# Optimization experiments

Hardware: AMD Instinct MI355X
Metric: run time of the kernel (lower is better)

## Reference

```python
import jax, jax.numpy as jnp
import numpy as np

# CODABlocks (codomain attention) with per_channel_attention=True:
# token_codimension = head_codimension = 1, scale = 2, n_modes = [32, 32],
# mixer_modes = [16, 16], temperature = 1.0, instance_norm (affine) everywhere.
N_HEADS = 16
TEMPERATURE = 1.0
EPS = 1e-5

def _gelu(z):
    return jax.nn.gelu(z, approximate=False)  # matches torch F.gelu default (erf)

def instance_norm(x, g, b):
    # x: (B, C, H, W); normalize over spatial dims per (sample, channel), affine.
    mu = jnp.mean(x, axis=(-2, -1), keepdims=True)
    var = jnp.var(x, axis=(-2, -1), keepdims=True)
    return (x - mu) * jax.lax.rsqrt(var + EPS) * g[:, None, None] + b[:, None, None]

def conv1x1(x, w, b):
    return jnp.einsum('bihw,io->bohw', x, w) + b[None, :, None, None]

def fourier_resample(x, out_shape):
    # FFT-based spatial resampling (mode truncation / zero-pad), norm='forward'.
    if tuple(x.shape[-2:]) == tuple(out_shape):
        return x
    Ho, Wo = out_shape
    xft = jnp.fft.rfftn(x, axes=(-2, -1), norm='forward')
    out = jnp.zeros(x.shape[:-2] + (Ho, Wo // 2 + 1), dtype=xft.dtype)
    hk = min(x.shape[-2], Ho) // 2
    wk = min(xft.shape[-1], Wo // 2 + 1)
    out = out.at[..., :hk, :wk].set(xft[..., :hk, :wk])
    out = out.at[..., -hk:, :wk].set(xft[..., -hk:, :wk])
    return jnp.fft.irfftn(out, s=out_shape, axes=(-2, -1), norm='forward')

def spectral_conv(x, w, out_shape):
    # Truncated-mode spectral convolution (dense weights, equiv. to tucker rank=1.0).
    # w: (Cin, Cout, 2*mh, mw, 2) -> complex weight on kept Fourier modes.
    wc = w[..., 0] + 1j * w[..., 1]
    mh = wc.shape[2] // 2
    mw = wc.shape[3]
    Ho, Wo = out_shape
    xft = jnp.fft.rfftn(x, axes=(-2, -1), norm='forward')   # (B, Cin, H, W//2+1)
    top = jnp.einsum('bihw,iohw->bohw', xft[:, :, :mh, :mw], wc[:, :, :mh])
    bot = jnp.einsum('bihw,iohw->bohw', xft[:, :, -mh:, :mw], wc[:, :, mh:])
    out_ft = jnp.zeros((x.shape[0], wc.shape[1], Ho, Wo // 2 + 1), dtype=xft.dtype)
    out_ft = out_ft.at[:, :, :mh, :mw].set(top)
    out_ft = out_ft.at[:, :, -mh:, :mw].set(bot)
    return jnp.fft.irfftn(out_ft, s=out_shape, axes=(-2, -1), norm='forward')

def fno_layer(x, spec_w, skip_w, skip_b, out_shape, norm=None, act=None):
    # One FNOBlocks layer: spectral conv + (resampled) linear skip, optional norm/act.
    xs = fourier_resample(conv1x1(x, skip_w, skip_b), out_shape)
    xf = spectral_conv(x, spec_w, out_shape)
    if norm is not None:
        xf = instance_norm(xf, *norm)
    y = xf + xs
    return act(y) if act is not None else y

def codano_forward(x, key_w, key_skip_w, key_skip_b, query_w, query_skip_w, query_skip_b, value_w, value_skip_w, value_skip_b, proj_w, proj_skip_w, proj_skip_b, norm1_g, norm1_b, attn_norm_g, attn_norm_b, norm2_g, norm2_b, mixer_w1, mixer_skip_w1, mixer_skip_b1, mixer_norm_g1, mixer_norm_b1, mixer_w2, mixer_skip_w2, mixer_skip_b2, mixer_norm_g2, mixer_norm_b2, mixer_out_g, mixer_out_b):
    b, t, H, W = x.shape   # token codim d = 1 -> channel dim == number of tokens
    tokens = x.reshape(b * t, 1, H, W)
    tokens_norm = instance_norm(tokens, norm1_g, norm1_b)
    Hs, Ws = H // 2, W // 2   # K, Q downsampled by scale = 2
    k = fno_layer(tokens_norm, key_w, key_skip_w, key_skip_b, (Hs, Ws))
    q = fno_layer(tokens_norm, query_w, query_skip_w, query_skip_b, (Hs, Ws))
    v = fno_layer(tokens_norm, value_w, value_skip_w, value_skip_b, (H, W))

    def heads_flat(z):
        hh, ww = z.shape[-2:]
        # (b*t, n_heads*d, h, w) -> (b, heads, t, d*h*w), d = 1
        return z.reshape(b, t, N_HEADS, hh * ww).transpose(0, 2, 1, 3)

    kf, qf, vf = heads_flat(k), heads_flat(q), heads_flat(v)
    scale = jnp.sqrt(jnp.asarray(kf.shape[-1], jnp.float32)) * TEMPERATURE
    dprod = jax.nn.softmax(jnp.einsum('bhtd,bhsd->bhts', qf, kf) / scale, axis=-1)
    attn = jnp.einsum('bhts,bhsd->bhtd', dprod, vf)      # (b, heads, t, H*W)
    attn = attn.transpose(0, 2, 1, 3).reshape(b * t, N_HEADS, H, W)
    # multi-head projection back to token codimension (n_heads -> 1)
    attn = fno_layer(attn, proj_w, proj_skip_w, proj_skip_b, (H, W))
    attn = instance_norm(attn + tokens, attn_norm_g, attn_norm_b)
    # permutation-equivariant mixer: 2 FNO layers shared across all tokens
    m = instance_norm(attn, norm2_g, norm2_b)
    m = fno_layer(m, mixer_w1, mixer_skip_w1, mixer_skip_b1, (H, W), norm=(mixer_norm_g1, mixer_norm_b1), act=_gelu)
    m = fno_layer(m, mixer_w2, mixer_skip_w2, mixer_skip_b2, (H, W), norm=(mixer_norm_g2, mixer_norm_b2))
    out = instance_norm(m, mixer_out_g, mixer_out_b) + attn
    return out.reshape(b, t, H, W)

def setup_inputs():
    key = jax.random.key(0)
    ks = list(jax.random.split(key, 32))
    f32 = jnp.float32
    def W_(k, shape, s=0.02):
        return (s * jax.random.normal(k, shape)).astype(f32)
    B, T, H, Wd = 4, 32, 128, 128
    mh_s, mw_s = 16, 9    # mixer_modes [16,16]: 2*(16//2) rows, 16//2+1 rfft cols
    mh_f, mw_f = 32, 17   # n_modes [32,32]
    return {
        'x': jax.random.normal(ks[0], (B, T, H, Wd), dtype=f32),
        'key_w': W_(ks[1], (1, N_HEADS, mh_s, mw_s, 2)),
        'key_skip_w': W_(ks[2], (1, N_HEADS), 0.5),
        'key_skip_b': W_(ks[3], (N_HEADS,)),
        'query_w': W_(ks[4], (1, N_HEADS, mh_s, mw_s, 2)),
        'query_skip_w': W_(ks[5], (1, N_HEADS), 0.5),
        'query_skip_b': W_(ks[6], (N_HEADS,)),
        'value_w': W_(ks[7], (1, N_HEADS, mh_s, mw_s, 2)),
        'value_skip_w': W_(ks[8], (1, N_HEADS), 0.5),
        'value_skip_b': W_(ks[9], (N_HEADS,)),
        'proj_w': W_(ks[10], (N_HEADS, 1, mh_f, mw_f, 2)),
        'proj_skip_w': W_(ks[11], (N_HEADS, 1), 0.25),
        'proj_skip_b': W_(ks[12], (1,)),
        'norm1_g': jnp.ones((1,), f32), 'norm1_b': jnp.zeros((1,), f32),
        'attn_norm_g': jnp.ones((1,), f32), 'attn_norm_b': jnp.zeros((1,), f32),
        'norm2_g': jnp.ones((1,), f32), 'norm2_b': jnp.zeros((1,), f32),
        'mixer_w1': W_(ks[13], (1, 1, mh_f, mw_f, 2)),
        'mixer_skip_w1': W_(ks[14], (1, 1), 0.5),
        'mixer_skip_b1': W_(ks[15], (1,)),
        'mixer_norm_g1': jnp.ones((1,), f32), 'mixer_norm_b1': jnp.zeros((1,), f32),
        'mixer_w2': W_(ks[16], (1, 1, mh_f, mw_f, 2)),
        'mixer_skip_w2': W_(ks[17], (1, 1), 0.5),
        'mixer_skip_b2': W_(ks[18], (1,)),
        'mixer_norm_g2': jnp.ones((1,), f32), 'mixer_norm_b2': jnp.zeros((1,), f32),
        'mixer_out_g': jnp.ones((1,), f32), 'mixer_out_b': jnp.zeros((1,), f32),
    }

def reference(x, key_w, key_skip_w, key_skip_b, query_w, query_skip_w, query_skip_b, value_w, value_skip_w, value_skip_b, proj_w, proj_skip_w, proj_skip_b, norm1_g, norm1_b, attn_norm_g, attn_norm_b, norm2_g, norm2_b, mixer_w1, mixer_skip_w1, mixer_skip_b1, mixer_norm_g1, mixer_norm_b1, mixer_w2, mixer_skip_w2, mixer_skip_b2, mixer_norm_g2, mixer_norm_b2, mixer_out_g, mixer_out_b):
    return codano_forward(x, key_w, key_skip_w, key_skip_b, query_w, query_skip_w, query_skip_b, value_w, value_skip_w, value_skip_b, proj_w, proj_skip_w, proj_skip_b, norm1_g, norm1_b, attn_norm_g, attn_norm_b, norm2_g, norm2_b, mixer_w1, mixer_skip_w1, mixer_skip_b1, mixer_norm_g1, mixer_norm_b1, mixer_w2, mixer_skip_w2, mixer_skip_b2, mixer_norm_g2, mixer_norm_b2, mixer_out_g, mixer_out_b)
```

## Files before the change

kernel.cpp:

```cpp
#include <hip/hip_runtime.h>
#include <cmath>

#define PI_F 3.14159265358979323846f
#define NTOK 128
#define NPIX 16384
#define NHEADS 16

__device__ __forceinline__ void block_reduce2(float& a, float& b){
  __shared__ float sa[4], sb[4];
  __syncthreads();
  for (int o=32;o>0;o>>=1){ a += __shfl_down(a,o); b += __shfl_down(b,o); }
  int w = threadIdx.x>>6, l = threadIdx.x&63;
  if (l==0){ sa[w]=a; sb[w]=b; }
  __syncthreads();
  a = sa[0]+sa[1]+sa[2]+sa[3];
  b = sb[0]+sb[1]+sb[2]+sb[3];
}

__device__ __forceinline__ float block_reduce1(float a){
  __shared__ float sa[4];
  __syncthreads();
  for (int o=32;o>0;o>>=1) a += __shfl_down(a,o);
  int w = threadIdx.x>>6, l = threadIdx.x&63;
  if (l==0) sa[w]=a;
  __syncthreads();
  return sa[0]+sa[1]+sa[2]+sa[3];
}

__device__ __forceinline__ float gelu_f(float y){
  return 0.5f*y*(1.f + erff(y*0.70710678118f));
}

__device__ __forceinline__ void affine_from(const float* __restrict__ ps, float g, float bb, int t,
                                            float& a, float& b0){
  float sum=0.f,sq=0.f;
  #pragma unroll
  for (int s=0;s<8;s++){ const float* p=ps+((size_t)t*8+s)*2; sum+=p[0]; sq+=p[1]; }
  const float iN=1.f/NPIX;
  float mu=sum*iN, var=sq*iN-mu*mu;
  a=rsqrtf(var+1e-5f)*g;
  b0=bb-mu*a;
}
__device__ __forceinline__ void scalA_from(const float* __restrict__ psA, float ag, float n2g, int t,
                                           float& muZ, float& aA, float& a0){
  float sum=0.f,sq=0.f;
  #pragma unroll
  for (int s=0;s<8;s++){ const float* p=psA+((size_t)t*8+s)*2; sum+=p[0]; sq+=p[1]; }
  const float iN=1.f/NPIX;
  muZ=sum*iN; float var=sq*iN-muZ*muZ;
  float inv=rsqrtf(var+1e-5f);
  aA=inv*ag;
  float var2=aA*aA*var;
  a0=aA*rsqrtf(var2+1e-5f)*n2g;
}
__device__ __forceinline__ void scalB_from(const float* __restrict__ psB, float mng1, int t,
                                           float& mu1, float& c1){
  float sum=0.f,sq=0.f;
  #pragma unroll
  for (int s=0;s<8;s++){ const float* p=psB+((size_t)t*8+s)*2; sum+=p[0]; sq+=p[1]; }
  const float iN=1.f/NPIX;
  mu1=sum*iN; float var=sq*iN-mu1*mu1;
  c1=rsqrtf(var+1e-5f)*mng1;
}
__device__ __forceinline__ void scalC_from(const float* __restrict__ psC, float mng2, float K, float sw,
                                           float outg, int t,
                                           float& mu2f, float& c2, float& mu3, float& c3){
  float sf=0.f,sfsq=0.f,sm=0.f,smsq=0.f,sx=0.f;
  #pragma unroll
  for (int s=0;s<8;s++){
    const float* p=psC+((size_t)t*8+s)*5;
    sf+=p[0]; sfsq+=p[1]; sm+=p[2]; smsq+=p[3]; sx+=p[4];
  }
  const float iN=1.f/NPIX;
  mu2f=sf*iN; float var2=sfsq*iN-mu2f*mu2f;
  c2=rsqrtf(var2+1e-5f)*mng2;
  float Em1=sm*iN, Em1sq=smsq*iN, Exm=sx*iN;
  float Em2=K+sw*Em1;
  float Em2sq = c2*c2*var2 + sw*sw*Em1sq + K*K
              + 2.f*c2*sw*(Exm - mu2f*Em1) + 2.f*K*sw*Em1;
  float var_m2=Em2sq-Em2*Em2;
  mu3=Em2;
  c3=rsqrtf(var_m2+1e-5f)*outg;
}

__global__ __launch_bounds__(256) void k_stats0(const float* __restrict__ x, float* __restrict__ pstat){
  int t=blockIdx.x, slab=blockIdx.y;
  const float* xs = x + (size_t)t*NPIX + slab*2048;
  float sum=0.f, sq=0.f;
  for (int i=threadIdx.x;i<2048;i+=256){ float v=xs[i]; sum+=v; sq+=v*v; }
  block_reduce2(sum,sq);
  if (threadIdx.x==0){ float* o=pstat+((size_t)t*8+slab)*2; o[0]=sum; o[1]=sq; }
}

__global__ __launch_bounds__(256) void k_colfft33(const float* __restrict__ x, const float* __restrict__ pstat0,
                          const float* __restrict__ n1g, const float* __restrict__ n1b,
                          float* __restrict__ A){
  __shared__ float rows[16*128];
  __shared__ float tw[128][2];
  int base = blockIdx.x*16;
  int t = base>>7;
  float a,b0; affine_from(pstat0, n1g[0], n1b[0], t, a, b0);
  for (int i=threadIdx.x;i<2048;i+=256) rows[i] = a*x[(size_t)base*128 + i] + b0;
  for (int p=threadIdx.x;p<128;p+=256){ float sn,cs; sincosf(-(2.f*PI_F/128.f)*(float)p,&sn,&cs); tw[p][0]=cs; tw[p][1]=sn; }
  __syncthreads();
  for (int e=threadIdx.x;e<16*33;e+=256){
    int r=e/33, c=e%33;
    const float* rp=rows+r*128;
    float re=0.f, im=0.f;
    for (int w=0;w<128;w++){
      int p=(c*w)&127;
      float v=rp[w];
      re+=v*tw[p][0]; im+=v*tw[p][1];
    }
    float* o=A+((size_t)(base+r)*33+c)*2; o[0]=re; o[1]=im;
  }
}

__global__ __launch_bounds__(256) void k_rowfft64(const float* __restrict__ A,
                          float* __restrict__ X64, float* __restrict__ X64h){
  int s=blockIdx.x, cg=blockIdx.y;
  int c0=cg*11;
  __shared__ float a[128][11][2];
  __shared__ float S[64][11][2];
  __shared__ float tw[128][2];
  for (int i=threadIdx.x;i<128*22;i+=256){
    int r=i/22, q=i%22;
    a[r][q>>1][q&1] = A[((size_t)(s*128+r)*33 + c0)*2 + q];
  }
  for (int p=threadIdx.x;p<128;p+=256){ float sn,cs; sincosf(-(2.f*PI_F/128.f)*(float)p,&sn,&cs); tw[p][0]=cs; tw[p][1]=sn; }
  __syncthreads();
  const float sc=1.f/16384.f;
  for (int e=threadIdx.x;e<64*11;e+=256){
    int i2=e/11, cl=e%11;
    int r=(i2<32)? i2 : i2+64;
    float re=0.f, im=0.f;
    for (int h=0;h<128;h++){
      int p=(r*h)&127;
      float cs=tw[p][0], sn=tw[p][1];
      float ar=a[h][cl][0], ai=a[h][cl][1];
      re+=ar*cs-ai*sn; im+=ar*sn+ai*cs;
    }
    S[i2][cl][0]=re*sc; S[i2][cl][1]=im*sc;
  }
  __syncthreads();
  for (int e=threadIdx.x;e<64*11;e+=256){
    int r=e/11, cl=e%11; int c=c0+cl;
    float vr=S[r][cl][0], vi=S[r][cl][1];
    float* o=X64+((size_t)s*(64*33)+r*33+c)*2; o[0]=vr; o[1]=vi;
    float hr=vr, hi=vi;
    if (c==0 || c==32){
      int pr=(64-r)&63;
      hr=0.5f*(vr+S[pr][cl][0]);
      hi=0.5f*(vi-S[pr][cl][1]);
    }
    float* oh=X64h+((size_t)s*(64*33)+r*33+c)*2; oh[0]=hr; oh[1]=hi;
  }
}

__global__ __launch_bounds__(256) void k_Ue(const float* __restrict__ X64h, float* __restrict__ Ue){
  int b=blockIdx.x, t=blockIdx.y, sg=blockIdx.z;
  __shared__ float2 xt[2112];
  const float2* src = (const float2*)(X64h + ((size_t)(b*32+t))*4224);
  for (int m=threadIdx.x;m<2112;m+=256){
    int r=m/33, c=m%33;
    bool excl = (c<=8) && (r<=8 || r>=56);
    float w = excl? 0.f : ((c==0||c==32)? 1.f : 2.f);
    float2 v = src[m];
    xt[m]=make_float2(v.x*w, v.y*w);
  }
  __syncthreads();
  float acc[4]={0.f,0.f,0.f,0.f};
  const float2* s0=(const float2*)(X64h + ((size_t)(b*32+sg*4))*4224);
  for (int m=threadIdx.x;m<2112;m+=256){
    float2 a2=xt[m];
    #pragma unroll
    for (int j=0;j<4;j++){
      float2 b2=s0[(size_t)j*2112+m];
      acc[j]+=a2.x*b2.x+a2.y*b2.y;
    }
  }
  for (int j=0;j<4;j++){
    float r=block_reduce1(acc[j]);
    if (threadIdx.x==0) Ue[((size_t)(b*32+t))*32 + sg*4+j]=r;
  }
}

__global__ __launch_bounds__(256) void k_ZYw(const float* __restrict__ X64, const float* __restrict__ X64h,
    const float* __restrict__ qw, const float* __restrict__ qsw,
    const float* __restrict__ kw, const float* __restrict__ ksw,
    const float* __restrict__ value_w, const float* __restrict__ vsw, const float* __restrict__ vsb,
    const float* __restrict__ proj_w, const float* __restrict__ psw,
    float* __restrict__ Zq, float* __restrict__ Zk, float* __restrict__ Yw){
  int t=blockIdx.x, h=blockIdx.y;
  __shared__ float Xs[1088];
  __shared__ float2 xh0[17];
  for (int e=threadIdx.x;e<544;e+=256){
    int j=e/17, c=e%17;
    int i2=(j<16)? j : (j+32);
    const float* xp = X64 + ((size_t)t*(64*33) + i2*33 + c)*2;
    Xs[e*2]=xp[0]; Xs[e*2+1]=xp[1];
  }
  if (threadIdx.x<17){
    int j=threadIdx.x;
    int r=(j<=8)? j : j+47;
    const float* hp = X64h + ((size_t)t*(64*33) + r*33)*2;
    xh0[j]=make_float2(hp[0],hp[1]);
  }
  __syncthreads();
  float aq=qsw[h], ak=ksw[h];
  for (int e=threadIdx.x;e<306;e+=256){
    int side=e/153, m=e%153;
    int j=m/9, c=m%9;
    int jj=(j<=8)? j : j+15;
    const float* W = side? kw : qw;
    float a = side? ak : aq;
    float prx=0.f, pry=0.f;
    if (j!=8){
      int jw=(j<8)? j : j-1;
      const float* wp = W + ((size_t)(h*16+jw)*9 + c)*2;
      float xrr=Xs[(jj*17+c)*2], xri=Xs[(jj*17+c)*2+1];
      prx = wp[0]*xrr - wp[1]*xri;
      pry = wp[0]*xri + wp[1]*xrr;
    }
    float Vx=prx, Vy=pry;
    if (c==0){
      int jp = (j==0)? 0 : 17-j;
      float ppx=0.f, ppy=0.f;
      if (jp!=8){
        int jw2=(jp<8)? jp : jp-1;
        const float* wp2 = W + ((size_t)(h*16+jw2)*9)*2;
        int jj2=(jp<=8)? jp : jp+15;
        float x2r=Xs[(jj2*17)*2], x2i=Xs[(jj2*17)*2+1];
        ppx = wp2[0]*x2r - wp2[1]*x2i;
        ppy = wp2[0]*x2i + wp2[1]*x2r;
      }
      Vx = 0.5f*(prx + ppx);
      Vy = 0.5f*(pry - ppy);
    }
    float xmr, xmi;
    if (c==0){ xmr=xh0[j].x; xmi=xh0[j].y; }
    else { xmr=Xs[(jj*17+c)*2]; xmi=Xs[(jj*17+c)*2+1]; }
    float zr = a*xmr + Vx;
    float zi = a*xmi + Vy;
    float wf = (side && c!=0)? 2.f : 1.f;
    float* dst = (side? Zk : Zq) + ((size_t)(t*16+h))*306 + m*2;
    dst[0]=wf*zr; dst[1]=wf*zi;
  }
  int b=t>>5, s=t&31;
  float vw=vsw[h], vb=vsb[h], pw=psw[h];
  size_t obase = ((size_t)(b*16+h)*32 + s)*1088;
  for (int e=threadIdx.x;e<544;e+=256){
    int j=e/17, c=e%17;
    float xr=Xs[e*2], xi=Xs[e*2+1];
    float wvr=0.f,wvi=0.f;
    if (c<=8 && (j<8||j>=24)){
      int jw=(j<8)? j : (j-16);
      const float* wv = value_w + ((size_t)(h*16+jw)*9 + c)*2;
      wvr=wv[0]; wvi=wv[1];
    }
    float Mr=xr*wvr-xi*wvi, Mi=xr*wvi+xi*wvr;
    float Mhr=Mr, Mhi=Mi;
    if (c==0){
      float Pr2=0.f,Pi2=0.f;
      int jp2=(j==0)?0:((j==16)?-1:32-j);
      if (jp2>=0 && (jp2<8||jp2>=24)){
        int jw2=(jp2<8)? jp2 : (jp2-16);
        const float* wv2=value_w+((size_t)(h*16+jw2)*9)*2;
        float pxr=Xs[(jp2*17)*2], pxi=Xs[(jp2*17)*2+1];
        Pr2=pxr*wv2[0]-pxi*wv2[1];
        Pi2=pxr*wv2[1]+pxi*wv2[0];
      }
      Mhr=0.5f*(Mr+Pr2); Mhi=0.5f*(Mi-Pi2);
    }
    float Yr=vw*xr+Mhr+((e==0)? vb:0.f);
    float Yi=vw*xi+Mhi;
    const float* pc=proj_w+((size_t)(h*32+j)*17+c)*2;
    float pr=pc[0], pi=pc[1];
    float* o=Yw+obase+e*2;
    o[0]=pr*Yr-pi*Yi+pw*Mr;
    o[1]=pr*Yi+pi*Yr+pw*Mi;
  }
}

__global__ __launch_bounds__(256) void k_scores2(const float* __restrict__ Zq, const float* __restrict__ Zk,
                          const float* __restrict__ Ue,
                          const float* __restrict__ qsw, const float* __restrict__ qsb,
                          const float* __restrict__ ksw, const float* __restrict__ ksb,
                          float* __restrict__ P){
  int b=blockIdx.x, h=blockIdx.y;
  __shared__ float2 zq[32][154];
  __shared__ float2 zk[16][154];
  __shared__ float Pl[32][33];
  for (int i=threadIdx.x;i<32*153;i+=256){
    int t=i/153, m=i%153;
    zq[t][m]=((const float2*)(Zq + ((size_t)((b*32+t)*16+h))*306))[m];
  }
  float aq=qsw[h], ak=ksw[h], bq=qsb[h], bk=ksb[h];
  float aqak=aq*ak;
  int t=threadIdx.x>>3, sl=threadIdx.x&7;
  for (int ch=0; ch<2; ch++){
    __syncthreads();
    for (int i=threadIdx.x;i<16*153;i+=256){
      int s=i/153, m=i%153;
      zk[s][m]=((const float2*)(Zk + ((size_t)((b*32+ch*16+s)*16+h))*306))[m];
    }
    __syncthreads();
    for (int u=0;u<2;u++){
      int sr = sl + u*8;
      int s = ch*16 + sr;
      float acc=0.f;
      for (int m=0;m<153;m++){
        float2 a2=zq[t][m], c2=zk[sr][m];
        acc += a2.x*c2.x + a2.y*c2.y;
      }
      float G = aqak*Ue[((size_t)(b*32+t))*32+s] + acc;
      Pl[t][s] = 64.f*(G + bk*zq[t][0].x + bq*zk[sr][0].x + bq*bk);
    }
  }
  __syncthreads();
  if (threadIdx.x<32){
    int tt=threadIdx.x;
    float mx=-INFINITY;
    for (int s=0;s<32;s++) mx=fmaxf(mx,Pl[tt][s]);
    float e[32]; float sum=0.f;
    for (int s=0;s<32;s++){ e[s]=expf(Pl[tt][s]-mx); sum+=e[s]; }
    float inv=1.f/sum;
    size_t base=((size_t)(b*16+h)*32+tt)*32;
    for (int s=0;s<32;s++) P[base+s]=e[s]*inv;
  }
}

__global__ __launch_bounds__(256) void k_SfC2(const float* __restrict__ P, const float* __restrict__ Yw,
        float* __restrict__ Sfp){
  int b=blockIdx.x, ec=blockIdx.y, g=blockIdx.z;
  int e0=ec*64, hs0=g*128;
  __shared__ float Pl[128][32];
  for (int i=threadIdx.x;i<128*32;i+=256){
    int hsl=i>>5, t=i&31;
    int hs=hs0+hsl, h=hs>>5, s=hs&31;
    Pl[hsl][t]=P[(((size_t)(b*16+h)*32)+t)*32+s];
  }
  __syncthreads();
  int el=threadIdx.x&63, tg=threadIdx.x>>6;
  float acc[8];
  #pragma unroll
  for (int j=0;j<8;j++) acc[j]=0.f;
  const float* Yb = Yw + ((size_t)b*512 + hs0)*1088 + e0 + el;
  #pragma unroll 4
  for (int hsl=0;hsl<128;hsl++){
    float y = Yb[(size_t)hsl*1088];
    #pragma unroll
    for (int j=0;j<8;j++) acc[j] += Pl[hsl][tg*8+j]*y;
  }
  #pragma unroll
  for (int j=0;j<8;j++){
    int t=tg*8+j;
    Sfp[((size_t)(b*32+t)*4+g)*1088 + e0 + el] = acc[j];
  }
}

__global__ __launch_bounds__(256) void k_skipmix(const float* __restrict__ x, const float* __restrict__ P,
                          const float* __restrict__ pw, const float* __restrict__ vw,
                          const float* __restrict__ pstat0, const float* __restrict__ n1g,
                          const float* __restrict__ n1b, float* __restrict__ out){
  int b=blockIdx.x, ch=blockIdx.y, tt=blockIdx.z;
  int pxb=ch*512;
  __shared__ float Rs[16][32];
  __shared__ float cbs[16];
  __shared__ float as2[32], b0s[32];
  if (threadIdx.x<32){
    float a,b0; affine_from(pstat0, n1g[0], n1b[0], b*32+threadIdx.x, a, b0);
    as2[threadIdx.x]=a; b0s[threadIdx.x]=b0;
  }
  __syncthreads();
  for (int rr=threadIdx.x; rr<512; rr+=256){
    int tl=rr>>5, s=rr&31;
    int t=tt*16+tl;
    float acc=0.f;
    for (int h=0;h<16;h++)
      acc += pw[h]*vw[h]*P[(((size_t)(b*16+h)*32)+t)*32+s];
    Rs[tl][s]=acc*as2[s];
    float cb=acc*b0s[s];
    for (int o=16;o>0;o>>=1) cb+=__shfl_down(cb,o,32);
    if (s==0) cbs[tl]=cb;
  }
  __syncthreads();
  float a0[16], a1[16];
  #pragma unroll
  for (int t=0;t<16;t++){ a0[t]=0.f; a1[t]=0.f; }
  for (int s=0;s<32;s++){
    const float* xp = x + ((size_t)(b*32+s))*NPIX + pxb;
    float v0=xp[threadIdx.x], v1=xp[threadIdx.x+256];
    #pragma unroll
    for (int t=0;t<16;t++){ float r=Rs[t][s]; a0[t]+=r*v0; a1[t]+=r*v1; }
  }
  #pragma unroll
  for (int t=0;t<16;t++){
    int gt=tt*16+t;
    float cb=cbs[t];
    float* op = out + ((size_t)(b*32+gt))*NPIX + pxb;
    op[threadIdx.x]=a0[t]+cb; op[threadIdx.x+256]=a1[t]+cb;
  }
}

__global__ __launch_bounds__(256) void k_field0(const float* __restrict__ Sfp,
        const float* __restrict__ sk, const float* __restrict__ x,
        const float* __restrict__ psw, const float* __restrict__ vsb, const float* __restrict__ psb,
        float* __restrict__ zf, float* __restrict__ pstatA){
  int bt = blockIdx.x, slab = blockIdx.y;
  __shared__ float Ss[1088];
  __shared__ float T[16*17*2];
  __shared__ float tw[128][2];
  for (int i=threadIdx.x;i<1088;i+=256){
    const float* sp4 = Sfp + (size_t)bt*4352 + i;
    Ss[i] = sp4[0]+sp4[1088]+sp4[2176]+sp4[3264];
  }
  for (int p=threadIdx.x;p<128;p+=256){ float sn,cs; sincosf((2.f*PI_F/128.f)*(float)p,&sn,&cs); tw[p][0]=cs; tw[p][1]=sn; }
  __syncthreads();
  int h0 = slab*16;
  for (int e=threadIdx.x;e<16*17;e+=256){
    int hl=e/17, c=e%17; int h=h0+hl;
    float re=0.f, im=0.f;
    for (int j=0;j<32;j++){
      int r=(j<16)? j : (j+96);
      int p=(r*h)&127;
      float cs=tw[p][0], sn=tw[p][1];
      float ar=Ss[(j*17+c)*2], ai=Ss[(j*17+c)*2+1];
      re += ar*cs - ai*sn;
      im += ar*sn + ai*cs;
    }
    T[e*2]=re; T[e*2+1]=im;
  }
  __syncthreads();
  size_t base = (size_t)bt*NPIX + h0*128;
  float Cb = psb[0];
  for (int hh=0;hh<16;hh++) Cb += psw[hh]*vsb[hh];
  float sum=0.f, sq=0.f;
  for (int pos=threadIdx.x;pos<2048;pos+=256){
    int hl=pos>>7, w=pos&127;
    const float* Th=T+hl*17*2;
    float br=tw[w][0], bi=tw[w][1];
    float rr=br, ri=bi;
    float v=Th[0];
    for (int c=1;c<17;c++){
      v += 2.f*(Th[c*2]*rr - Th[c*2+1]*ri);
      float nr=rr*br-ri*bi; ri=rr*bi+ri*br; rr=nr;
    }
    float val = v + sk[base+pos] + x[base+pos] + Cb;
    zf[base+pos]=val; sum+=val; sq+=val*val;
  }
  block_reduce2(sum,sq);
  if (threadIdx.x==0){ float* o=pstatA+((size_t)bt*8+slab)*2; o[0]=sum; o[1]=sq; }
}

__global__ __launch_bounds__(256) void k_specm0(const float* __restrict__ P,
    const float* __restrict__ pw, const float* __restrict__ vw,
    const float* __restrict__ Sfp, const float* __restrict__ X64,
    const float* __restrict__ pstat0, const float* __restrict__ pstatA,
    const float* __restrict__ n1g, const float* __restrict__ n1b,
    const float* __restrict__ ag, const float* __restrict__ n2g, const float* __restrict__ n2b,
    const float* __restrict__ psw, const float* __restrict__ vsb, const float* __restrict__ psb,
    float* __restrict__ sp){
  int bt=blockIdx.x; int b=bt>>5, t=bt&31;
  __shared__ float Rs[32];
  __shared__ float Sfl[1088];
  if (threadIdx.x<32){
    int s=threadIdx.x; float acc=0.f;
    for (int h=0;h<16;h++)
      acc += pw[h]*vw[h]*P[(((size_t)(b*16+h)*32)+t)*32+s];
    Rs[s]=acc;
  }
  for (int i=threadIdx.x;i<1088;i+=256){
    const float* sp4 = Sfp + (size_t)bt*4352 + i;
    Sfl[i]=sp4[0]+sp4[1088]+sp4[2176]+sp4[3264];
  }
  __syncthreads();
  float a_t,b0_t; affine_from(pstat0,n1g[0],n1b[0],bt,a_t,b0_t);
  float muZ,aA,a0; scalA_from(pstatA,ag[0],n2g[0],bt,muZ,aA,a0);
  float Cb=psb[0];
  for (int h=0;h<16;h++) Cb+=psw[h]*vsb[h];
  float inva=1.f/a_t;
  for (int e=threadIdx.x;e<544;e+=256){
    int j=e/17, c=e%17;
    float sr=Sfl[e*2], si=Sfl[e*2+1];
    if (c==0){
      if (j==0){ si=0.f; }
      else if (j==16){ sr*=0.5f; si*=0.5f; }
      else { int jp=32-j; sr=0.5f*(sr+Sfl[jp*34]); si=0.5f*(si-Sfl[jp*34+1]); }
    }
    int i2=(j<16)? j : (j+32);
    float re=0.f, im=0.f;
    const float* xb = X64 + ((size_t)(b*32)*(64*33) + i2*33 + c)*2;
    for (int s=0;s<32;s++){
      const float* xp = xb + (size_t)s*(64*33)*2;
      float r=Rs[s];
      re += r*xp[0]; im += r*xp[1];
    }
    const float* xt = X64 + ((size_t)bt*(64*33) + i2*33 + c)*2;
    re += inva*xt[0]; im += inva*xt[1];
    float zr=sr+re, zi=si+im;
    if (e==0) zr += Cb - b0_t*inva;
    float mr=a0*zr, mi=a0*zi;
    if (e==0) mr += n2b[0] - muZ*a0;
    sp[((size_t)bt*544+e)*2]=mr; sp[((size_t)bt*544+e)*2+1]=mi;
  }
}

__global__ __launch_bounds__(256) void k_field1(const float* __restrict__ sp, const float* __restrict__ wm,
        float* __restrict__ fd1, float* __restrict__ pstatB){
  int bt = blockIdx.x, slab = blockIdx.y;
  __shared__ float Ss[1088];
  __shared__ float T[16*17*2];
  __shared__ float tw[128][2];
  for (int e=threadIdx.x;e<544;e+=256){
    float xr=sp[((size_t)bt*544+e)*2], xi=sp[((size_t)bt*544+e)*2+1];
    float wr=wm[e*2], wi=wm[e*2+1];
    Ss[e*2]=xr*wr-xi*wi; Ss[e*2+1]=xr*wi+xi*wr;
  }
  for (int p=threadIdx.x;p<128;p+=256){ float sn,cs; sincosf((2.f*PI_F/128.f)*(float)p,&sn,&cs); tw[p][0]=cs; tw[p][1]=sn; }
  __syncthreads();
  int h0 = slab*16;
  for (int e=threadIdx.x;e<16*17;e+=256){
    int hl=e/17, c=e%17; int h=h0+hl;
    float re=0.f, im=0.f;
    for (int j=0;j<32;j++){
      int r=(j<16)? j : (j+96);
      int p=(r*h)&127;
      float cs=tw[p][0], sn=tw[p][1];
      float ar=Ss[(j*17+c)*2], ai=Ss[(j*17+c)*2+1];
      re += ar*cs - ai*sn;
      im += ar*sn + ai*cs;
    }
    T[e*2]=re; T[e*2+1]=im;
  }
  __syncthreads();
  size_t base = (size_t)bt*NPIX + h0*128;
  float sum=0.f, sq=0.f;
  for (int pos=threadIdx.x;pos<2048;pos+=256){
    int hl=pos>>7, w=pos&127;
    const float* Th=T+hl*17*2;
    float br=tw[w][0], bi=tw[w][1];
    float rr=br, ri=bi;
    float v=Th[0];
    for (int c=1;c<17;c++){
      v += 2.f*(Th[c*2]*rr - Th[c*2+1]*ri);
      float nr=rr*br-ri*bi; ri=rr*bi+ri*br; rr=nr;
    }
    fd1[base+pos]=v; sum+=v; sq+=v*v;
  }
  block_reduce2(sum,sq);
  if (threadIdx.x==0){ float* o=pstatB+((size_t)bt*8+slab)*2; o[0]=sum; o[1]=sq; }
}

__global__ __launch_bounds__(256) void k_colA1(const float* __restrict__ f1, const float* __restrict__ z,
        const float* __restrict__ pstatA, const float* __restrict__ pstatB,
        const float* __restrict__ ag, const float* __restrict__ n2g, const float* __restrict__ mng1,
        const float* __restrict__ n2b,
        const float* __restrict__ mnb1, const float* __restrict__ msw1, const float* __restrict__ msb1,
        float* __restrict__ A){
  __shared__ float rows[16*128];
  __shared__ float tw[128][2];
  int grow = blockIdx.x*16;
  int t = grow>>7;
  float muZ,aA,a0;
  scalA_from(pstatA, ag[0], n2g[0], t, muZ, aA, a0);
  float b2 = n2b[0];
  float mu1,c1;
  scalB_from(pstatB, mng1[0], t, mu1, c1);
  float nb=mnb1[0], sw=msw1[0], sb=msb1[0];
  for (int i=threadIdx.x;i<2048;i+=256){
    size_t gi=(size_t)grow*128+i;
    float m0v=(z[gi]-muZ)*a0+b2;
    float y=(f1[gi]-mu1)*c1+nb + m0v*sw + sb;
    rows[i]=gelu_f(y);
  }
  for (int p=threadIdx.x;p<128;p+=256){ float sn,cs; sincosf(-(2.f*PI_F/128.f)*(float)p,&sn,&cs); tw[p][0]=cs; tw[p][1]=sn; }
  __syncthreads();
  for (int e=threadIdx.x;e<16*17;e+=256){
    int r=e/17, c=e%17;
    const float* rp=rows+r*128;
    float re=0.f, im=0.f;
    for (int w=0;w<128;w++){
      int p=(c*w)&127;
      float v=rp[w];
      re+=v*tw[p][0]; im+=v*tw[p][1];
    }
    float* o=A+((size_t)(grow+r)*17+c)*2; o[0]=re; o[1]=im;
  }
}

__global__ __launch_bounds__(256) void k_rowfft32(const float* __restrict__ A, float* __restrict__ spec){
  int s=blockIdx.x, cg=blockIdx.y;
  int c0 = (cg==0)? 0 : (1+cg*4);
  int nc = (cg==0)? 5 : 4;
  __shared__ float a[128*5*2];
  __shared__ float tw[128][2];
  for (int i=threadIdx.x;i<128*nc*2;i+=256){
    int r=i/(2*nc), q=i%(2*nc);
    a[(r*5+(q>>1))*2+(q&1)] = A[((size_t)(s*128+r)*17 + c0)*2 + q];
  }
  for (int p=threadIdx.x;p<128;p+=256){ float sn,cs; sincosf(-(2.f*PI_F/128.f)*(float)p,&sn,&cs); tw[p][0]=cs; tw[p][1]=sn; }
  __syncthreads();
  const float sc=1.f/16384.f;
  for (int e=threadIdx.x;e<32*nc;e+=256){
    int j=e/nc, cl=e%nc;
    int r=(j<16)? j : (j+96);
    float re=0.f,im=0.f;
    for (int h=0;h<128;h++){
      int p=(r*h)&127;
      float cs=tw[p][0], sn=tw[p][1];
      float ar=a[(h*5+cl)*2], ai=a[(h*5+cl)*2+1];
      re += ar*cs - ai*sn;
      im += ar*sn + ai*cs;
    }
    float* o=spec+((size_t)s*544 + j*17 + c0+cl)*2;
    o[0]=re*sc; o[1]=im*sc;
  }
}

__global__ __launch_bounds__(256) void k_field2(const float* __restrict__ sp2, const float* __restrict__ wm,
        const float* __restrict__ f1, const float* __restrict__ z,
        const float* __restrict__ pstatA, const float* __restrict__ pstatB,
        const float* __restrict__ ag, const float* __restrict__ n2g, const float* __restrict__ mng1,
        const float* __restrict__ n2b, const float* __restrict__ mnb1,
        const float* __restrict__ msw1, const float* __restrict__ msb1,
        float* __restrict__ fd2, float* __restrict__ pstatC){
  int bt = blockIdx.x, slab = blockIdx.y;
  __shared__ float Ss[1088];
  __shared__ float T[16*17*2];
  __shared__ float tw[128][2];
  for (int e=threadIdx.x;e<544;e+=256){
    float xr=sp2[((size_t)bt*544+e)*2], xi=sp2[((size_t)bt*544+e)*2+1];
    float wr=wm[e*2], wi=wm[e*2+1];
    Ss[e*2]=xr*wr-xi*wi; Ss[e*2+1]=xr*wi+xi*wr;
  }
  for (int p=threadIdx.x;p<128;p+=256){ float sn,cs; sincosf((2.f*PI_F/128.f)*(float)p,&sn,&cs); tw[p][0]=cs; tw[p][1]=sn; }
  __syncthreads();
  int h0 = slab*16;
  for (int e=threadIdx.x;e<16*17;e+=256){
    int hl=e/17, c=e%17; int h=h0+hl;
    float re=0.f, im=0.f;
    for (int j=0;j<32;j++){
      int r=(j<16)? j : (j+96);
      int p=(r*h)&127;
      float cs=tw[p][0], sn=tw[p][1];
      float ar=Ss[(j*17+c)*2], ai=Ss[(j*17+c)*2+1];
      re += ar*cs - ai*sn;
      im += ar*sn + ai*cs;
    }
    T[e*2]=re; T[e*2+1]=im;
  }
  __syncthreads();
  size_t base = (size_t)bt*NPIX + h0*128;
  float muZ,aA,a0,mu1,c1;
  scalA_from(pstatA, ag[0], n2g[0], bt, muZ, aA, a0);
  scalB_from(pstatB, mng1[0], bt, mu1, c1);
  float b2=n2b[0], nb1=mnb1[0], sw1=msw1[0], sb1=msb1[0];
  float s_f=0.f,s_fsq=0.f,s_m=0.f,s_msq=0.f,s_x=0.f;
  for (int pos=threadIdx.x;pos<2048;pos+=256){
    int hl=pos>>7, w=pos&127;
    const float* Th=T+hl*17*2;
    float br=tw[w][0], bi=tw[w][1];
    float rr=br, ri=bi;
    float v=Th[0];
    for (int c=1;c<17;c++){
      v += 2.f*(Th[c*2]*rr - Th[c*2+1]*ri);
      float nr=rr*br-ri*bi; ri=rr*bi+ri*br; rr=nr;
    }
    size_t gi=base+pos;
    float m0v=(z[gi]-muZ)*a0+b2;
    float y=(f1[gi]-mu1)*c1+nb1 + m0v*sw1 + sb1;
    float m1v=gelu_f(y);
    fd2[gi]=v;
    s_f+=v; s_fsq+=v*v; s_m+=m1v; s_msq+=m1v*m1v; s_x+=v*m1v;
  }
  block_reduce2(s_f,s_fsq);
  block_reduce2(s_m,s_msq);
  s_x = block_reduce1(s_x);
  if (threadIdx.x==0){
    float* o=pstatC+((size_t)bt*8+slab)*5;
    o[0]=s_f; o[1]=s_fsq; o[2]=s_m; o[3]=s_msq; o[4]=s_x;
  }
}

__global__ __launch_bounds__(256) void k_final2(const float* __restrict__ z, const float* __restrict__ f1,
        const float* __restrict__ f2,
        const float* __restrict__ pstatA, const float* __restrict__ pstatB, const float* __restrict__ pstatC,
        const float* __restrict__ ag, const float* __restrict__ n2g, const float* __restrict__ mng1,
        const float* __restrict__ mng2, const float* __restrict__ outg,
        const float* __restrict__ ab, const float* __restrict__ n2b,
        const float* __restrict__ mnb1, const float* __restrict__ msw1, const float* __restrict__ msb1,
        const float* __restrict__ mnb2, const float* __restrict__ msw2, const float* __restrict__ msb2,
        const float* __restrict__ outb, float* __restrict__ out){
  int bt=blockIdx.x, slab=blockIdx.y;
  float muZ,aA,a0,mu1,c1,mu2f,c2,mu3,c3;
  scalA_from(pstatA, ag[0], n2g[0], bt, muZ, aA, a0);
  scalB_from(pstatB, mng1[0], bt, mu1, c1);
  float sw2=msw2[0], K=mnb2[0]+msb2[0];
  scalC_from(pstatC, mng2[0], K, sw2, outg[0], bt, mu2f, c2, mu3, c3);
  float b1=ab[0], b2=n2b[0], nb1=mnb1[0], sw1=msw1[0], sb1=msb1[0];
  float nb2=mnb2[0], sb2=msb2[0], bo=outb[0];
  size_t base=(size_t)bt*NPIX + (size_t)slab*2048;
  for (int i=threadIdx.x;i<2048;i+=256){
    size_t gi=base+i;
    float zv=z[gi];
    float m0v=(zv-muZ)*a0+b2;
    float a2v=(zv-muZ)*aA+b1;
    float y=(f1[gi]-mu1)*c1+nb1 + m0v*sw1 + sb1;
    float m1v=gelu_f(y);
    float m2v=(f2[gi]-mu2f)*c2+nb2 + m1v*sw2 + sb2;
    out[gi]=(m2v-mu3)*c3+bo+a2v;
  }
}

extern "C" void kernel_launch(void* const* d_in, const int* in_sizes, int n_in,
                              void* d_out, int out_size, void* d_ws, size_t ws_size,
                              hipStream_t stream){
  const float* x        = (const float*)d_in[0];
  const float* key_w    = (const float*)d_in[1];
  const float* key_sw   = (const float*)d_in[2];
  const float* key_sb   = (const float*)d_in[3];
  const float* query_w  = (const float*)d_in[4];
  const float* query_sw = (const float*)d_in[5];
  const float* query_sb = (const float*)d_in[6];
  const float* value_w  = (const float*)d_in[7];
  const float* value_sw = (const float*)d_in[8];
  const float* value_sb = (const float*)d_in[9];
  const float* proj_w   = (const float*)d_in[10];
  const float* proj_sw  = (const float*)d_in[11];
  const float* proj_sb  = (const float*)d_in[12];
  const float* norm1_g  = (const float*)d_in[13];
  const float* norm1_b  = (const float*)d_in[14];
  const float* attn_g   = (const float*)d_in[15];
  const float* attn_b   = (const float*)d_in[16];
  const float* norm2_g  = (const float*)d_in[17];
  const float* norm2_b  = (const float*)d_in[18];
  const float* mw1      = (const float*)d_in[19];
  const float* msw1     = (const float*)d_in[20];
  const float* msb1     = (const float*)d_in[21];
  const float* mng1     = (const float*)d_in[22];
  const float* mnb1     = (const float*)d_in[23];
  const float* mw2      = (const float*)d_in[24];
  const float* msw2     = (const float*)d_in[25];
  const float* msb2     = (const float*)d_in[26];
  const float* mng2     = (const float*)d_in[27];
  const float* mnb2     = (const float*)d_in[28];
  const float* outg     = (const float*)d_in[29];
  const float* outb     = (const float*)d_in[30];
  float* out = (float*)d_out;
  float* ws  = (float*)d_ws;

  size_t off=0;
  float* A   = ws + off; off += (size_t)128*128*33*2;
  float* X64 = ws + off; off += (size_t)128*64*33*2;
  float* X64h= ws + off; off += (size_t)128*64*33*2;
  float* Zq  = ws + off; off += (size_t)128*16*306;
  float* Zk  = ws + off; off += (size_t)128*16*306;
  float* Ue  = ws + off; off += (size_t)4*32*32;
  float* P   = ws + off; off += (size_t)4*16*32*32;
  float* Yw  = ws + off; off += (size_t)2048*1088;
  float* Sfp = ws + off; off += (size_t)128*4*1088;
  float* sk  = ws + off; off += (size_t)128*16384;
  float* zf  = ws + off; off += (size_t)128*16384;
  float* fd1 = ws + off; off += (size_t)128*16384;
  float* fd2 = ws + off; off += (size_t)128*16384;
  float* sp  = ws + off; off += (size_t)128*544*2;
  float* sp2 = ws + off; off += (size_t)128*544*2;
  float* pstat0 = ws + off; off += (size_t)128*8*2;
  float* pstatA = ws + off; off += (size_t)128*8*2;
  float* pstatB = ws + off; off += (size_t)128*8*2;
  float* pstatC = ws + off; off += (size_t)128*8*5;

  k_stats0<<<dim3(128,8),256,0,stream>>>(x, pstat0);
  k_colfft33<<<1024,256,0,stream>>>(x, pstat0, norm1_g, norm1_b, A);
  k_rowfft64<<<dim3(128,3),256,0,stream>>>(A, X64, X64h);
  k_Ue<<<dim3(4,32,8),256,0,stream>>>(X64h, Ue);
  k_ZYw<<<dim3(128,16),256,0,stream>>>(X64, X64h, query_w, query_sw, key_w, key_sw,
      value_w, value_sw, value_sb, proj_w, proj_sw, Zq, Zk, Yw);
  k_scores2<<<dim3(4,16),256,0,stream>>>(Zq, Zk, Ue, query_sw, query_sb, key_sw, key_sb, P);
  k_SfC2<<<dim3(4,17,4),256,0,stream>>>(P, Yw, Sfp);
  k_skipmix<<<dim3(4,32,2),256,0,stream>>>(x, P, proj_sw, value_sw, pstat0, norm1_g, norm1_b, sk);

  k_field0<<<dim3(128,8),256,0,stream>>>(Sfp, sk, x, proj_sw, value_sb, proj_sb, zf, pstatA);
  k_specm0<<<128,256,0,stream>>>(P, proj_sw, value_sw, Sfp, X64, pstat0, pstatA,
      norm1_g, norm1_b, attn_g, norm2_g, norm2_b, proj_sw, value_sb, proj_sb, sp);
  k_field1<<<dim3(128,8),256,0,stream>>>(sp, mw1, fd1, pstatB);
  k_colA1<<<1024,256,0,stream>>>(fd1, zf, pstatA, pstatB, attn_g, norm2_g, mng1,
      norm2_b, mnb1, msw1, msb1, A);
  k_rowfft32<<<dim3(128,4),256,0,stream>>>(A, sp2);
  k_field2<<<dim3(128,8),256,0,stream>>>(sp2, mw2, fd1, zf, pstatA, pstatB,
      attn_g, norm2_g, mng1, norm2_b, mnb1, msw1, msb1, fd2, pstatC);
  k_final2<<<dim3(128,8),256,0,stream>>>(zf, fd1, fd2, pstatA, pstatB, pstatC,
      attn_g, norm2_g, mng1, mng2, outg, attn_b, norm2_b,
      mnb1, msw1, msb1, mnb2, msw2, msb2, outb, out);
}
```

Measured before the change: 333.2 us.

## Merge independent kernels into combined launches and split field kernels finer

```diff
diff --git a/kernel.cpp b/kernel.cpp
--- a/kernel.cpp
+++ b/kernel.cpp
@@ -45,7 +45,7 @@
                                            float& muZ, float& aA, float& a0){
   float sum=0.f,sq=0.f;
   #pragma unroll
-  for (int s=0;s<8;s++){ const float* p=psA+((size_t)t*8+s)*2; sum+=p[0]; sq+=p[1]; }
+  for (int s=0;s<16;s++){ const float* p=psA+((size_t)t*16+s)*2; sum+=p[0]; sq+=p[1]; }
   const float iN=1.f/NPIX;
   muZ=sum*iN; float var=sq*iN-muZ*muZ;
   float inv=rsqrtf(var+1e-5f);
@@ -57,7 +57,7 @@
                                            float& mu1, float& c1){
   float sum=0.f,sq=0.f;
   #pragma unroll
-  for (int s=0;s<8;s++){ const float* p=psB+((size_t)t*8+s)*2; sum+=p[0]; sq+=p[1]; }
+  for (int s=0;s<16;s++){ const float* p=psB+((size_t)t*16+s)*2; sum+=p[0]; sq+=p[1]; }
   const float iN=1.f/NPIX;
   mu1=sum*iN; float var=sq*iN-mu1*mu1;
   c1=rsqrtf(var+1e-5f)*mng1;
@@ -67,8 +67,8 @@
                                            float& mu2f, float& c2, float& mu3, float& c3){
   float sf=0.f,sfsq=0.f,sm=0.f,smsq=0.f,sx=0.f;
   #pragma unroll
-  for (int s=0;s<8;s++){
-    const float* p=psC+((size_t)t*8+s)*5;
+  for (int s=0;s<16;s++){
+    const float* p=psC+((size_t)t*16+s)*5;
     sf+=p[0]; sfsq+=p[1]; sm+=p[2]; smsq+=p[3]; sx+=p[4];
   }
   const float iN=1.f/NPIX;
@@ -157,128 +157,132 @@
   }
 }
 
-__global__ __launch_bounds__(256) void k_Ue(const float* __restrict__ X64h, float* __restrict__ Ue){
-  int b=blockIdx.x, t=blockIdx.y, sg=blockIdx.z;
-  __shared__ float2 xt[2112];
-  const float2* src = (const float2*)(X64h + ((size_t)(b*32+t))*4224);
-  for (int m=threadIdx.x;m<2112;m+=256){
-    int r=m/33, c=m%33;
-    bool excl = (c<=8) && (r<=8 || r>=56);
-    float w = excl? 0.f : ((c==0||c==32)? 1.f : 2.f);
-    float2 v = src[m];
-    xt[m]=make_float2(v.x*w, v.y*w);
-  }
-  __syncthreads();
-  float acc[4]={0.f,0.f,0.f,0.f};
-  const float2* s0=(const float2*)(X64h + ((size_t)(b*32+sg*4))*4224);
-  for (int m=threadIdx.x;m<2112;m+=256){
-    float2 a2=xt[m];
-    #pragma unroll
-    for (int j=0;j<4;j++){
-      float2 b2=s0[(size_t)j*2112+m];
-      acc[j]+=a2.x*b2.x+a2.y*b2.y;
-    }
-  }
-  for (int j=0;j<4;j++){
-    float r=block_reduce1(acc[j]);
-    if (threadIdx.x==0) Ue[((size_t)(b*32+t))*32 + sg*4+j]=r;
-  }
-}
-
-__global__ __launch_bounds__(256) void k_ZYw(const float* __restrict__ X64, const float* __restrict__ X64h,
+__global__ __launch_bounds__(256) void k_UeZYw(const float* __restrict__ X64, const float* __restrict__ X64h,
     const float* __restrict__ qw, const float* __restrict__ qsw,
     const float* __restrict__ kw, const float* __restrict__ ksw,
     const float* __restrict__ value_w, const float* __restrict__ vsw, const float* __restrict__ vsb,
     const float* __restrict__ proj_w, const float* __restrict__ psw,
-    float* __restrict__ Zq, float* __restrict__ Zk, float* __restrict__ Yw){
-  int t=blockIdx.x, h=blockIdx.y;
-  __shared__ float Xs[1088];
-  __shared__ float2 xh0[17];
-  for (int e=threadIdx.x;e<544;e+=256){
-    int j=e/17, c=e%17;
-    int i2=(j<16)? j : (j+32);
-    const float* xp = X64 + ((size_t)t*(64*33) + i2*33 + c)*2;
-    Xs[e*2]=xp[0]; Xs[e*2+1]=xp[1];
-  }
-  if (threadIdx.x<17){
-    int j=threadIdx.x;
-    int r=(j<=8)? j : j+47;
-    const float* hp = X64h + ((size_t)t*(64*33) + r*33)*2;
-    xh0[j]=make_float2(hp[0],hp[1]);
-  }
-  __syncthreads();
-  float aq=qsw[h], ak=ksw[h];
-  for (int e=threadIdx.x;e<306;e+=256){
-    int side=e/153, m=e%153;
-    int j=m/9, c=m%9;
-    int jj=(j<=8)? j : j+15;
-    const float* W = side? kw : qw;
-    float a = side? ak : aq;
-    float prx=0.f, pry=0.f;
-    if (j!=8){
-      int jw=(j<8)? j : j-1;
-      const float* wp = W + ((size_t)(h*16+jw)*9 + c)*2;
-      float xrr=Xs[(jj*17+c)*2], xri=Xs[(jj*17+c)*2+1];
-      prx = wp[0]*xrr - wp[1]*xri;
-      pry = wp[0]*xri + wp[1]*xrr;
-    }
-    float Vx=prx, Vy=pry;
-    if (c==0){
-      int jp = (j==0)? 0 : 17-j;
-      float ppx=0.f, ppy=0.f;
-      if (jp!=8){
-        int jw2=(jp<8)? jp : jp-1;
-        const float* wp2 = W + ((size_t)(h*16+jw2)*9)*2;
-        int jj2=(jp<=8)? jp : jp+15;
-        float x2r=Xs[(jj2*17)*2], x2i=Xs[(jj2*17)*2+1];
-        ppx = wp2[0]*x2r - wp2[1]*x2i;
-        ppy = wp2[0]*x2i + wp2[1]*x2r;
+    float* __restrict__ Zq, float* __restrict__ Zk, float* __restrict__ Yw,
+    float* __restrict__ Ue){
+  __shared__ float sh[4224];
+  int bx=blockIdx.x;
+  if (bx<2048){
+    int t=bx>>4, h=bx&15;
+    float* Xs = sh;
+    float2* xh0 = (float2*)(sh+1092);
+    for (int e=threadIdx.x;e<544;e+=256){
+      int j=e/17, c=e%17;
+      int i2=(j<16)? j : (j+32);
+      const float* xp = X64 + ((size_t)t*(64*33) + i2*33 + c)*2;
+      Xs[e*2]=xp[0]; Xs[e*2+1]=xp[1];
+    }
+    if (threadIdx.x<17){
+      int j=threadIdx.x;
+      int r=(j<=8)? j : j+47;
+      const float* hp = X64h + ((size_t)t*(64*33) + r*33)*2;
+      xh0[j]=make_float2(hp[0],hp[1]);
+    }
+    __syncthreads();
+    float aq=qsw[h], ak=ksw[h];
+    for (int e=threadIdx.x;e<306;e+=256){
+      int side=e/153, m=e%153;
+      int j=m/9, c=m%9;
+      int jj=(j<=8)? j : j+15;
+      const float* W = side? kw : qw;
+      float a = side? ak : aq;
+      float prx=0.f, pry=0.f;
+      if (j!=8){
+        int jw=(j<8)? j : j-1;
+        const float* wp = W + ((size_t)(h*16+jw)*9 + c)*2;
+        float xrr=Xs[(jj*17+c)*2], xri=Xs[(jj*17+c)*2+1];
+        prx = wp[0]*xrr - wp[1]*xri;
+        pry = wp[0]*xri + wp[1]*xrr;
       }
-      Vx = 0.5f*(prx + ppx);
-      Vy = 0.5f*(pry - ppy);
-    }
-    float xmr, xmi;
-    if (c==0){ xmr=xh0[j].x; xmi=xh0[j].y; }
-    else { xmr=Xs[(jj*17+c)*2]; xmi=Xs[(jj*17+c)*2+1]; }
-    float zr = a*xmr + Vx;
-    float zi = a*xmi + Vy;
-    float wf = (side && c!=0)? 2.f : 1.f;
-    float* dst = (side? Zk : Zq) + ((size_t)(t*16+h))*306 + m*2;
-    dst[0]=wf*zr; dst[1]=wf*zi;
-  }
-  int b=t>>5, s=t&31;
-  float vw=vsw[h], vb=vsb[h], pw=psw[h];
-  size_t obase = ((size_t)(b*16+h)*32 + s)*1088;
-  for (int e=threadIdx.x;e<544;e+=256){
-    int j=e/17, c=e%17;
-    float xr=Xs[e*2], xi=Xs[e*2+1];
-    float wvr=0.f,wvi=0.f;
-    if (c<=8 && (j<8||j>=24)){
-      int jw=(j<8)? j : (j-16);
-      const float* wv = value_w + ((size_t)(h*16+jw)*9 + c)*2;
-      wvr=wv[0]; wvi=wv[1];
-    }
-    float Mr=xr*wvr-xi*wvi, Mi=xr*wvi+xi*wvr;
-    float Mhr=Mr, Mhi=Mi;
-    if (c==0){
-      float Pr2=0.f,Pi2=0.f;
-      int jp2=(j==0)?0:((j==16)?-1:32-j);
-      if (jp2>=0 && (jp2<8||jp2>=24)){
-        int jw2=(jp2<8)? jp2 : (jp2-16);
-        const float* wv2=value_w+((size_t)(h*16+jw2)*9)*2;
-        float pxr=Xs[(jp2*17)*2], pxi=Xs[(jp2*17)*2+1];
-        Pr2=pxr*wv2[0]-pxi*wv2[1];
-        Pi2=pxr*wv2[1]+pxi*wv2[0];
+      float Vx=prx, Vy=pry;
+      if (c==0){
+        int jp = (j==0)? 0 : 17-j;
+        float ppx=0.f, ppy=0.f;
+        if (jp!=8){
+          int jw2=(jp<8)? jp : jp-1;
+          const float* wp2 = W + ((size_t)(h*16+jw2)*9)*2;
+          int jj2=(jp<=8)? jp : jp+15;
+          float x2r=Xs[(jj2*17)*2], x2i=Xs[(jj2*17)*2+1];
+          ppx = wp2[0]*x2r - wp2[1]*x2i;
+          ppy = wp2[0]*x2i + wp2[1]*x2r;
+        }
+        Vx = 0.5f*(prx + ppx);
+        Vy = 0.5f*(pry - ppy);
       }
-      Mhr=0.5f*(Mr+Pr2); Mhi=0.5f*(Mi-Pi2);
-    }
-    float Yr=vw*xr+Mhr+((e==0)? vb:0.f);
-    float Yi=vw*xi+Mhi;
-    const float* pc=proj_w+((size_t)(h*32+j)*17+c)*2;
-    float pr=pc[0], pi=pc[1];
-    float* o=Yw+obase+e*2;
-    o[0]=pr*Yr-pi*Yi+pw*Mr;
-    o[1]=pr*Yi+pi*Yr+pw*Mi;
+      float xmr, xmi;
+      if (c==0){ xmr=xh0[j].x; xmi=xh0[j].y; }
+      else { xmr=Xs[(jj*17+c)*2]; xmi=Xs[(jj*17+c)*2+1]; }
+      float zr = a*xmr + Vx;
+      float zi = a*xmi + Vy;
+      float wf = (side && c!=0)? 2.f : 1.f;
+      float* dst = (side? Zk : Zq) + ((size_t)(t*16+h))*306 + m*2;
+      dst[0]=wf*zr; dst[1]=wf*zi;
+    }
+    int b=t>>5, s=t&31;
+    float vw=vsw[h], vb=vsb[h], pw=psw[h];
+    size_t obase = ((size_t)(b*16+h)*32 + s)*1088;
+    for (int e=threadIdx.x;e<544;e+=256){
+      int j=e/17, c=e%17;
+      float xr=Xs[e*2], xi=Xs[e*2+1];
+      float wvr=0.f,wvi=0.f;
+      if (c<=8 && (j<8||j>=24)){
+        int jw=(j<8)? j : (j-16);
+        const float* wv = value_w + ((size_t)(h*16+jw)*9 + c)*2;
+        wvr=wv[0]; wvi=wv[1];
+      }
+      float Mr=xr*wvr-xi*wvi, Mi=xr*wvi+xi*wvr;
+      float Mhr=Mr, Mhi=Mi;
+      if (c==0){
+        float Pr2=0.f,Pi2=0.f;
+        int jp2=(j==0)?0:((j==16)?-1:32-j);
+        if (jp2>=0 && (jp2<8||jp2>=24)){
+          int jw2=(jp2<8)? jp2 : (jp2-16);
+          const float* wv2=value_w+((size_t)(h*16+jw2)*9)*2;
+          float pxr=Xs[(jp2*17)*2], pxi=Xs[(jp2*17)*2+1];
+          Pr2=pxr*wv2[0]-pxi*wv2[1];
+          Pi2=pxr*wv2[1]+pxi*wv2[0];
+        }
+        Mhr=0.5f*(Mr+Pr2); Mhi=0.5f*(Mi-Pi2);
+      }
+      float Yr=vw*xr+Mhr+((e==0)? vb:0.f);
+      float Yi=vw*xi+Mhi;
+      const float* pc=proj_w+((size_t)(h*32+j)*17+c)*2;
+      float pr=pc[0], pi=pc[1];
+      float* o=Yw+obase+e*2;
+      o[0]=pr*Yr-pi*Yi+pw*Mr;
+      o[1]=pr*Yi+pi*Yr+pw*Mi;
+    }
+  } else {
+    int u=bx-2048;
+    int b=u>>8, rem=u&255, t=rem>>3, sg=rem&7;
+    float2* xt=(float2*)sh;
+    const float2* src = (const float2*)(X64h + ((size_t)(b*32+t))*4224);
+    for (int m=threadIdx.x;m<2112;m+=256){
+      int r=m/33, c=m%33;
+      bool excl = (c<=8) && (r<=8 || r>=56);
+      float w = excl? 0.f : ((c==0||c==32)? 1.f : 2.f);
+      float2 v = src[m];
+      xt[m]=make_float2(v.x*w, v.y*w);
+    }
+    __syncthreads();
+    float acc[4]={0.f,0.f,0.f,0.f};
+    const float2* s0=(const float2*)(X64h + ((size_t)(b*32+sg*4))*4224);
+    for (int m=threadIdx.x;m<2112;m+=256){
+      float2 a2=xt[m];
+      #pragma unroll
+      for (int j=0;j<4;j++){
+        float2 b2=s0[(size_t)j*2112+m];
+        acc[j]+=a2.x*b2.x+a2.y*b2.y;
+      }
+    }
+    for (int j=0;j<4;j++){
+      float r=block_reduce1(acc[j]);
+      if (threadIdx.x==0) Ue[((size_t)(b*32+t))*32 + sg*4+j]=r;
+    }
   }
 }
 
@@ -287,17 +291,17 @@
                           const float* __restrict__ qsw, const float* __restrict__ qsb,
                           const float* __restrict__ ksw, const float* __restrict__ ksb,
                           float* __restrict__ P){
-  int b=blockIdx.x, h=blockIdx.y;
-  __shared__ float2 zq[32][154];
+  int b=blockIdx.x, h=blockIdx.y, tz=blockIdx.z;
+  __shared__ float2 zq[16][154];
   __shared__ float2 zk[16][154];
-  __shared__ float Pl[32][33];
-  for (int i=threadIdx.x;i<32*153;i+=256){
+  __shared__ float Pl[16][33];
+  for (int i=threadIdx.x;i<16*153;i+=256){
     int t=i/153, m=i%153;
-    zq[t][m]=((const float2*)(Zq + ((size_t)((b*32+t)*16+h))*306))[m];
+    zq[t][m]=((const float2*)(Zq + ((size_t)((b*32+tz*16+t)*16+h))*306))[m];
   }
   float aq=qsw[h], ak=ksw[h], bq=qsb[h], bk=ksb[h];
   float aqak=aq*ak;
-  int t=threadIdx.x>>3, sl=threadIdx.x&7;
+  int tl=threadIdx.x>>4, sl=threadIdx.x&15;
   for (int ch=0; ch<2; ch++){
     __syncthreads();
     for (int i=threadIdx.x;i<16*153;i+=256){
@@ -305,101 +309,102 @@
       zk[s][m]=((const float2*)(Zk + ((size_t)((b*32+ch*16+s)*16+h))*306))[m];
     }
     __syncthreads();
-    for (int u=0;u<2;u++){
-      int sr = sl + u*8;
-      int s = ch*16 + sr;
-      float acc=0.f;
-      for (int m=0;m<153;m++){
-        float2 a2=zq[t][m], c2=zk[sr][m];
-        acc += a2.x*c2.x + a2.y*c2.y;
-      }
-      float G = aqak*Ue[((size_t)(b*32+t))*32+s] + acc;
-      Pl[t][s] = 64.f*(G + bk*zq[t][0].x + bq*zk[sr][0].x + bq*bk);
-    }
-  }
-  __syncthreads();
-  if (threadIdx.x<32){
+    float acc=0.f;
+    for (int m=0;m<153;m++){
+      float2 a2=zq[tl][m], c2=zk[sl][m];
+      acc += a2.x*c2.x + a2.y*c2.y;
+    }
+    int s=ch*16+sl;
+    float G = aqak*Ue[((size_t)(b*32+tz*16+tl))*32+s] + acc;
+    Pl[tl][s] = 64.f*(G + bk*zq[tl][0].x + bq*zk[sl][0].x + bq*bk);
+  }
+  __syncthreads();
+  if (threadIdx.x<16){
     int tt=threadIdx.x;
     float mx=-INFINITY;
     for (int s=0;s<32;s++) mx=fmaxf(mx,Pl[tt][s]);
     float e[32]; float sum=0.f;
     for (int s=0;s<32;s++){ e[s]=expf(Pl[tt][s]-mx); sum+=e[s]; }
     float inv=1.f/sum;
-    size_t base=((size_t)(b*16+h)*32+tt)*32;
+    size_t base=((size_t)(b*16+h)*32+tz*16+tt)*32;
     for (int s=0;s<32;s++) P[base+s]=e[s]*inv;
   }
 }
 
-__global__ __launch_bounds__(256) void k_SfC2(const float* __restrict__ P, const float* __restrict__ Yw,
-        float* __restrict__ Sfp){
-  int b=blockIdx.x, ec=blockIdx.y, g=blockIdx.z;
-  int e0=ec*64, hs0=g*128;
-  __shared__ float Pl[128][32];
-  for (int i=threadIdx.x;i<128*32;i+=256){
-    int hsl=i>>5, t=i&31;
-    int hs=hs0+hsl, h=hs>>5, s=hs&31;
-    Pl[hsl][t]=P[(((size_t)(b*16+h)*32)+t)*32+s];
-  }
-  __syncthreads();
-  int el=threadIdx.x&63, tg=threadIdx.x>>6;
-  float acc[8];
-  #pragma unroll
-  for (int j=0;j<8;j++) acc[j]=0.f;
-  const float* Yb = Yw + ((size_t)b*512 + hs0)*1088 + e0 + el;
-  #pragma unroll 4
-  for (int hsl=0;hsl<128;hsl++){
-    float y = Yb[(size_t)hsl*1088];
+__global__ __launch_bounds__(256) void k_SfSk(const float* __restrict__ x, const float* __restrict__ P,
+        const float* __restrict__ Yw,
+        const float* __restrict__ pw, const float* __restrict__ vw,
+        const float* __restrict__ pstat0, const float* __restrict__ n1g, const float* __restrict__ n1b,
+        float* __restrict__ Sfp, float* __restrict__ sk){
+  __shared__ float sh[4096];
+  int bx=blockIdx.x;
+  if (bx<272){
+    int b=bx/68, rem=bx%68, ec=rem/4, g=rem%4;
+    int e0=ec*64, hs0=g*128;
+    float (*Pl)[32] = (float(*)[32])sh;
+    for (int i=threadIdx.x;i<128*32;i+=256){
+      int hsl=i>>5, t=i&31;
+      int hs=hs0+hsl, h=hs>>5, s=hs&31;
+      Pl[hsl][t]=P[(((size_t)(b*16+h)*32)+t)*32+s];
+    }
+    __syncthreads();
+    int el=threadIdx.x&63, tg=threadIdx.x>>6;
+    float acc[8];
     #pragma unroll
-    for (int j=0;j<8;j++) acc[j] += Pl[hsl][tg*8+j]*y;
-  }
-  #pragma unroll
-  for (int j=0;j<8;j++){
-    int t=tg*8+j;
-    Sfp[((size_t)(b*32+t)*4+g)*1088 + e0 + el] = acc[j];
-  }
-}
-
-__global__ __launch_bounds__(256) void k_skipmix(const float* __restrict__ x, const float* __restrict__ P,
-                          const float* __restrict__ pw, const float* __restrict__ vw,
-                          const float* __restrict__ pstat0, const float* __restrict__ n1g,
-                          const float* __restrict__ n1b, float* __restrict__ out){
-  int b=blockIdx.x, ch=blockIdx.y, tt=blockIdx.z;
-  int pxb=ch*512;
-  __shared__ float Rs[16][32];
-  __shared__ float cbs[16];
-  __shared__ float as2[32], b0s[32];
-  if (threadIdx.x<32){
-    float a,b0; affine_from(pstat0, n1g[0], n1b[0], b*32+threadIdx.x, a, b0);
-    as2[threadIdx.x]=a; b0s[threadIdx.x]=b0;
-  }
-  __syncthreads();
-  for (int rr=threadIdx.x; rr<512; rr+=256){
-    int tl=rr>>5, s=rr&31;
-    int t=tt*16+tl;
-    float acc=0.f;
-    for (int h=0;h<16;h++)
-      acc += pw[h]*vw[h]*P[(((size_t)(b*16+h)*32)+t)*32+s];
-    Rs[tl][s]=acc*as2[s];
-    float cb=acc*b0s[s];
-    for (int o=16;o>0;o>>=1) cb+=__shfl_down(cb,o,32);
-    if (s==0) cbs[tl]=cb;
-  }
-  __syncthreads();
-  float a0[16], a1[16];
-  #pragma unroll
-  for (int t=0;t<16;t++){ a0[t]=0.f; a1[t]=0.f; }
-  for (int s=0;s<32;s++){
-    const float* xp = x + ((size_t)(b*32+s))*NPIX + pxb;
-    float v0=xp[threadIdx.x], v1=xp[threadIdx.x+256];
+    for (int j=0;j<8;j++) acc[j]=0.f;
+    const float* Yb = Yw + ((size_t)b*512 + hs0)*1088 + e0 + el;
+    #pragma unroll 4
+    for (int hsl=0;hsl<128;hsl++){
+      float y = Yb[(size_t)hsl*1088];
+      #pragma unroll
+      for (int j=0;j<8;j++) acc[j] += Pl[hsl][tg*8+j]*y;
+    }
     #pragma unroll
-    for (int t=0;t<16;t++){ float r=Rs[t][s]; a0[t]+=r*v0; a1[t]+=r*v1; }
-  }
-  #pragma unroll
-  for (int t=0;t<16;t++){
-    int gt=tt*16+t;
-    float cb=cbs[t];
-    float* op = out + ((size_t)(b*32+gt))*NPIX + pxb;
-    op[threadIdx.x]=a0[t]+cb; op[threadIdx.x+256]=a1[t]+cb;
+    for (int j=0;j<8;j++){
+      int t=tg*8+j;
+      Sfp[((size_t)(b*32+t)*4+g)*1088 + e0 + el] = acc[j];
+    }
+  } else {
+    int u=bx-272;
+    int b=u>>6, rem=u&63, ch=rem>>1, tt=rem&1;
+    int pxb=ch*512;
+    float* Rs = sh;
+    float* cbs = sh+512;
+    float* as2 = sh+528;
+    float* b0s = sh+560;
+    if (threadIdx.x<32){
+      float a,b0; affine_from(pstat0, n1g[0], n1b[0], b*32+threadIdx.x, a, b0);
+      as2[threadIdx.x]=a; b0s[threadIdx.x]=b0;
+    }
+    __syncthreads();
+    for (int rr=threadIdx.x; rr<512; rr+=256){
+      int tl=rr>>5, s=rr&31;
+      int t=tt*16+tl;
+      float acc=0.f;
+      for (int h=0;h<16;h++)
+        acc += pw[h]*vw[h]*P[(((size_t)(b*16+h)*32)+t)*32+s];
+      Rs[tl*32+s]=acc*as2[s];
+      float cb=acc*b0s[s];
+      for (int o=16;o>0;o>>=1) cb+=__shfl_down(cb,o,32);
+      if (s==0) cbs[tl]=cb;
+    }
+    __syncthreads();
+    float a0[16], a1[16];
+    #pragma unroll
+    for (int t=0;t<16;t++){ a0[t]=0.f; a1[t]=0.f; }
+    for (int s=0;s<32;s++){
+      const float* xp = x + ((size_t)(b*32+s))*NPIX + pxb;
+      float v0=xp[threadIdx.x], v1=xp[threadIdx.x+256];
+      #pragma unroll
+      for (int t=0;t<16;t++){ float r=Rs[t*32+s]; a0[t]+=r*v0; a1[t]+=r*v1; }
+    }
+    #pragma unroll
+    for (int t=0;t<16;t++){
+      int gt=tt*16+t;
+      float cb=cbs[t];
+      float* op = sk + ((size_t)(b*32+gt))*NPIX + pxb;
+      op[threadIdx.x]=a0[t]+cb; op[threadIdx.x+256]=a1[t]+cb;
+    }
   }
 }
 
@@ -409,7 +414,7 @@
         float* __restrict__ zf, float* __restrict__ pstatA){
   int bt = blockIdx.x, slab = blockIdx.y;
   __shared__ float Ss[1088];
-  __shared__ float T[16*17*2];
+  __shared__ float T[8*17*2];
   __shared__ float tw[128][2];
   for (int i=threadIdx.x;i<1088;i+=256){
     const float* sp4 = Sfp + (size_t)bt*4352 + i;
@@ -417,8 +422,8 @@
   }
   for (int p=threadIdx.x;p<128;p+=256){ float sn,cs; sincosf((2.f*PI_F/128.f)*(float)p,&sn,&cs); tw[p][0]=cs; tw[p][1]=sn; }
   __syncthreads();
-  int h0 = slab*16;
-  for (int e=threadIdx.x;e<16*17;e+=256){
+  int h0 = slab*8;
+  for (int e=threadIdx.x;e<8*17;e+=256){
     int hl=e/17, c=e%17; int h=h0+hl;
     float re=0.f, im=0.f;
     for (int j=0;j<32;j++){
@@ -436,7 +441,7 @@
   float Cb = psb[0];
   for (int hh=0;hh<16;hh++) Cb += psw[hh]*vsb[hh];
   float sum=0.f, sq=0.f;
-  for (int pos=threadIdx.x;pos<2048;pos+=256){
+  for (int pos=threadIdx.x;pos<1024;pos+=256){
     int hl=pos>>7, w=pos&127;
     const float* Th=T+hl*17*2;
     float br=tw[w][0], bi=tw[w][1];
@@ -450,7 +455,7 @@
     zf[base+pos]=val; sum+=val; sq+=val*val;
   }
   block_reduce2(sum,sq);
-  if (threadIdx.x==0){ float* o=pstatA+((size_t)bt*8+slab)*2; o[0]=sum; o[1]=sq; }
+  if (threadIdx.x==0){ float* o=pstatA+((size_t)bt*16+slab)*2; o[0]=sum; o[1]=sq; }
 }
 
 __global__ __launch_bounds__(256) void k_specm0(const float* __restrict__ P,
@@ -461,7 +466,7 @@
     const float* __restrict__ ag, const float* __restrict__ n2g, const float* __restrict__ n2b,
     const float* __restrict__ psw, const float* __restrict__ vsb, const float* __restrict__ psb,
     float* __restrict__ sp){
-  int bt=blockIdx.x; int b=bt>>5, t=bt&31;
+  int bt=blockIdx.x, ec=blockIdx.y; int b=bt>>5, t=bt&31;
   __shared__ float Rs[32];
   __shared__ float Sfl[1088];
   if (threadIdx.x<32){
@@ -480,7 +485,8 @@
   float Cb=psb[0];
   for (int h=0;h<16;h++) Cb+=psw[h]*vsb[h];
   float inva=1.f/a_t;
-  for (int e=threadIdx.x;e<544;e+=256){
+  int e1=ec*272, e2=e1+272;
+  for (int e=e1+threadIdx.x;e<e2;e+=256){
     int j=e/17, c=e%17;
     float sr=Sfl[e*2], si=Sfl[e*2+1];
     if (c==0){
@@ -510,7 +516,7 @@
         float* __restrict__ fd1, float* __restrict__ pstatB){
   int bt = blockIdx.x, slab = blockIdx.y;
   __shared__ float Ss[1088];
-  __shared__ float T[16*17*2];
+  __shared__ float T[8*17*2];
   __shared__ float tw[128][2];
   for (int e=threadIdx.x;e<544;e+=256){
     float xr=sp[((size_t)bt*544+e)*2], xi=sp[((size_t)bt*544+e)*2+1];
@@ -519,8 +525,8 @@
   }
   for (int p=threadIdx.x;p<128;p+=256){ float sn,cs; sincosf((2.f*PI_F/128.f)*(float)p,&sn,&cs); tw[p][0]=cs; tw[p][1]=sn; }
   __syncthreads();
-  int h0 = slab*16;
-  for (int e=threadIdx.x;e<16*17;e+=256){
+  int h0 = slab*8;
+  for (int e=threadIdx.x;e<8*17;e+=256){
     int hl=e/17, c=e%17; int h=h0+hl;
     float re=0.f, im=0.f;
     for (int j=0;j<32;j++){
@@ -536,7 +542,7 @@
   __syncthreads();
   size_t base = (size_t)bt*NPIX + h0*128;
   float sum=0.f, sq=0.f;
-  for (int pos=threadIdx.x;pos<2048;pos+=256){
+  for (int pos=threadIdx.x;pos<1024;pos+=256){
     int hl=pos>>7, w=pos&127;
     const float* Th=T+hl*17*2;
     float br=tw[w][0], bi=tw[w][1];
@@ -549,7 +555,7 @@
     fd1[base+pos]=v; sum+=v; sq+=v*v;
   }
   block_reduce2(sum,sq);
-  if (threadIdx.x==0){ float* o=pstatB+((size_t)bt*8+slab)*2; o[0]=sum; o[1]=sq; }
+  if (threadIdx.x==0){ float* o=pstatB+((size_t)bt*16+slab)*2; o[0]=sum; o[1]=sq; }
 }
 
 __global__ __launch_bounds__(256) void k_colA1(const float* __restrict__ f1, const float* __restrict__ z,
@@ -627,7 +633,7 @@
         float* __restrict__ fd2, float* __restrict__ pstatC){
   int bt = blockIdx.x, slab = blockIdx.y;
   __shared__ float Ss[1088];
-  __shared__ float T[16*17*2];
+  __shared__ float T[8*17*2];
   __shared__ float tw[128][2];
   for (int e=threadIdx.x;e<544;e+=256){
     float xr=sp2[((size_t)bt*544+e)*2], xi=sp2[((size_t)bt*544+e)*2+1];
@@ -636,8 +642,8 @@
   }
   for (int p=threadIdx.x;p<128;p+=256){ float sn,cs; sincosf((2.f*PI_F/128.f)*(float)p,&sn,&cs); tw[p][0]=cs; tw[p][1]=sn; }
   __syncthreads();
-  int h0 = slab*16;
-  for (int e=threadIdx.x;e<16*17;e+=256){
+  int h0 = slab*8;
+  for (int e=threadIdx.x;e<8*17;e+=256){
     int hl=e/17, c=e%17; int h=h0+hl;
     float re=0.f, im=0.f;
     for (int j=0;j<32;j++){
@@ -657,7 +663,7 @@
   scalB_from(pstatB, mng1[0], bt, mu1, c1);
   float b2=n2b[0], nb1=mnb1[0], sw1=msw1[0], sb1=msb1[0];
   float s_f=0.f,s_fsq=0.f,s_m=0.f,s_msq=0.f,s_x=0.f;
-  for (int pos=threadIdx.x;pos<2048;pos+=256){
+  for (int pos=threadIdx.x;pos<1024;pos+=256){
     int hl=pos>>7, w=pos&127;
     const float* Th=T+hl*17*2;
     float br=tw[w][0], bi=tw[w][1];
@@ -678,7 +684,7 @@
   block_reduce2(s_m,s_msq);
   s_x = block_reduce1(s_x);
   if (threadIdx.x==0){
-    float* o=pstatC+((size_t)bt*8+slab)*5;
+    float* o=pstatC+((size_t)bt*16+slab)*5;
     o[0]=s_f; o[1]=s_fsq; o[2]=s_m; o[3]=s_msq; o[4]=s_x;
   }
 }
@@ -700,8 +706,8 @@
   scalC_from(pstatC, mng2[0], K, sw2, outg[0], bt, mu2f, c2, mu3, c3);
   float b1=ab[0], b2=n2b[0], nb1=mnb1[0], sw1=msw1[0], sb1=msb1[0];
   float nb2=mnb2[0], sb2=msb2[0], bo=outb[0];
-  size_t base=(size_t)bt*NPIX + (size_t)slab*2048;
-  for (int i=threadIdx.x;i<2048;i+=256){
+  size_t base=(size_t)bt*NPIX + (size_t)slab*1024;
+  for (int i=threadIdx.x;i<1024;i+=256){
     size_t gi=base+i;
     float zv=z[gi];
     float m0v=(zv-muZ)*a0+b2;
@@ -767,30 +773,28 @@
   float* sp  = ws + off; off += (size_t)128*544*2;
   float* sp2 = ws + off; off += (size_t)128*544*2;
   float* pstat0 = ws + off; off += (size_t)128*8*2;
-  float* pstatA = ws + off; off += (size_t)128*8*2;
-  float* pstatB = ws + off; off += (size_t)128*8*2;
-  float* pstatC = ws + off; off += (size_t)128*8*5;
+  float* pstatA = ws + off; off += (size_t)128*16*2;
+  float* pstatB = ws + off; off += (size_t)128*16*2;
+  float* pstatC = ws + off; off += (size_t)128*16*5;
 
   k_stats0<<<dim3(128,8),256,0,stream>>>(x, pstat0);
   k_colfft33<<<1024,256,0,stream>>>(x, pstat0, norm1_g, norm1_b, A);
   k_rowfft64<<<dim3(128,3),256,0,stream>>>(A, X64, X64h);
-  k_Ue<<<dim3(4,32,8),256,0,stream>>>(X64h, Ue);
-  k_ZYw<<<dim3(128,16),256,0,stream>>>(X64, X64h, query_w, query_sw, key_w, key_sw,
-      value_w, value_sw, value_sb, proj_w, proj_sw, Zq, Zk, Yw);
-  k_scores2<<<dim3(4,16),256,0,stream>>>(Zq, Zk, Ue, query_sw, query_sb, key_sw, key_sb, P);
-  k_SfC2<<<dim3(4,17,4),256,0,stream>>>(P, Yw, Sfp);
-  k_skipmix<<<dim3(4,32,2),256,0,stream>>>(x, P, proj_sw, value_sw, pstat0, norm1_g, norm1_b, sk);
-
-  k_field0<<<dim3(128,8),256,0,stream>>>(Sfp, sk, x, proj_sw, value_sb, proj_sb, zf, pstatA);
-  k_specm0<<<128,256,0,stream>>>(P, proj_sw, value_sw, Sfp, X64, pstat0, pstatA,
+  k_UeZYw<<<3072,256,0,stream>>>(X64, X64h, query_w, query_sw, key_w, key_sw,
+      value_w, value_sw, value_sb, proj_w, proj_sw, Zq, Zk, Yw, Ue);
+  k_scores2<<<dim3(4,16,2),256,0,stream>>>(Zq, Zk, Ue, query_sw, query_sb, key_sw, key_sb, P);
+  k_SfSk<<<528,256,0,stream>>>(x, P, Yw, proj_sw, value_sw, pstat0, norm1_g, norm1_b, Sfp, sk);
+
+  k_field0<<<dim3(128,16),256,0,stream>>>(Sfp, sk, x, proj_sw, value_sb, proj_sb, zf, pstatA);
+  k_specm0<<<dim3(128,2),256,0,stream>>>(P, proj_sw, value_sw, Sfp, X64, pstat0, pstatA,
       norm1_g, norm1_b, attn_g, norm2_g, norm2_b, proj_sw, value_sb, proj_sb, sp);
-  k_field1<<<dim3(128,8),256,0,stream>>>(sp, mw1, fd1, pstatB);
+  k_field1<<<dim3(128,16),256,0,stream>>>(sp, mw1, fd1, pstatB);
   k_colA1<<<1024,256,0,stream>>>(fd1, zf, pstatA, pstatB, attn_g, norm2_g, mng1,
       norm2_b, mnb1, msw1, msb1, A);
   k_rowfft32<<<dim3(128,4),256,0,stream>>>(A, sp2);
-  k_field2<<<dim3(128,8),256,0,stream>>>(sp2, mw2, fd1, zf, pstatA, pstatB,
+  k_field2<<<dim3(128,16),256,0,stream>>>(sp2, mw2, fd1, zf, pstatA, pstatB,
       attn_g, norm2_g, mng1, norm2_b, mnb1, msw1, msb1, fd2, pstatC);
-  k_final2<<<dim3(128,8),256,0,stream>>>(zf, fd1, fd2, pstatA, pstatB, pstatC,
+  k_final2<<<dim3(128,16),256,0,stream>>>(zf, fd1, fd2, pstatA, pstatB, pstatC,
       attn_g, norm2_g, mng1, mng2, outg, attn_b, norm2_b,
       mnb1, msw1, msb1, mnb2, msw2, msb2, outb, out);
 }
```

Measured after the change: 307.6 us. 7.7% less time.
